# Kernel optimization log

Hardware: AMD Instinct MI355X
Metric: run time of the kernel (lower is better)

Reference implementation:

```python
import jax, jax.numpy as jnp
import numpy as np

M, K, N = 4096, 4096, 11008  # tokens, in_features, out_features


def setup_inputs() -> dict:
    key = jax.random.key(0)
    k1, k2, k3, k4 = jax.random.split(key, 4)
    x = jax.random.normal(k1, (M, K), dtype=jnp.float32)
    weight = jax.random.randint(k2, (N, K), -128, 128).astype(jnp.int8)
    # per-output-channel scale, small positive values as from real quantization
    weight_scale = (jax.random.uniform(k3, (N,), dtype=jnp.float32) * 0.01 + 1e-4)
    bias = jax.random.normal(k4, (N,), dtype=jnp.float32)
    return {"x": x, "weight": weight, "weight_scale": weight_scale, "bias": bias}


def reference(x, weight, weight_scale, bias):
    # Dynamic per-token symmetric quantization of activations to int8.
    x_scale = jnp.max(jnp.abs(x), axis=-1, keepdims=True) / 127.0  # [M, 1]
    x_scale = jnp.maximum(x_scale, 1e-8)
    x_q = jnp.clip(jnp.round(x / x_scale), -128, 127).astype(jnp.int8)  # [M, K]
    acc = jax.lax.dot_general(
        x_q, weight,
        dimension_numbers=(((1,), (1,)), ((), ())),
        preferred_element_type=jnp.int32,
    )
    # Dequantize: per-token activation scale * per-channel weight scale, add bias.
    out = acc.astype(jnp.float32) * x_scale * weight_scale[None, :] + bias[None, :]
    return out
```

## Files before the change

kernel.cpp:

```cpp
#include <hip/hip_runtime.h>
#include <stdint.h>

#define M_DIM 4096
#define K_DIM 4096
#define N_DIM 11008

typedef int v4i __attribute__((ext_vector_type(4)));

#define LDSP(p) ((__attribute__((address_space(3))) void*)(uintptr_t)(p))
#define GLBP(p) ((__attribute__((address_space(1))) void*)(uintptr_t)(p))

__global__ __launch_bounds__(256) void quant_rows(const float* __restrict__ x,
                                                  int8_t* __restrict__ xq,
                                                  float* __restrict__ xs_out) {
    const int row = blockIdx.x;
    const int t = threadIdx.x;
    const float4* xr = (const float4*)(x + (size_t)row * K_DIM);

    float4 v[4];
    float amax = 0.0f;
#pragma unroll
    for (int r = 0; r < 4; ++r) {
        v[r] = xr[t + r * 256];
        amax = fmaxf(amax, fmaxf(fmaxf(fabsf(v[r].x), fabsf(v[r].y)),
                                 fmaxf(fabsf(v[r].z), fabsf(v[r].w))));
    }
#pragma unroll
    for (int off = 32; off > 0; off >>= 1)
        amax = fmaxf(amax, __shfl_xor(amax, off));

    __shared__ float smax[4];
    if ((t & 63) == 0) smax[t >> 6] = amax;
    __syncthreads();
    amax = fmaxf(fmaxf(smax[0], smax[1]), fmaxf(smax[2], smax[3]));

    const float xs = fmaxf(amax / 127.0f, 1e-8f);
    if (t == 0) xs_out[row] = xs;

    int* qo = (int*)(xq + (size_t)row * K_DIM);
#pragma unroll
    for (int r = 0; r < 4; ++r) {
        int q0 = (int)rintf(v[r].x / xs);
        int q1 = (int)rintf(v[r].y / xs);
        int q2 = (int)rintf(v[r].z / xs);
        int q3 = (int)rintf(v[r].w / xs);
        q0 = min(127, max(-128, q0));
        q1 = min(127, max(-128, q1));
        q2 = min(127, max(-128, q2));
        q3 = min(127, max(-128, q3));
        int packed = (q0 & 255) | ((q1 & 255) << 8) | ((q2 & 255) << 16) | (q3 << 24);
        qo[t + r * 256] = packed;
    }
}

__global__ __launch_bounds__(256) void prep_weight(const void* __restrict__ wraw,
                                                   int8_t* __restrict__ w8) {
    const int* wi = (const int*)wraw;
    int c = 0;
#pragma unroll
    for (int i = 0; i < 64; ++i) {
        int w = wi[i];
        c += (w >= -128 && w <= 127) ? 1 : 0;
    }
    const size_t tid = (size_t)blockIdx.x * 256 + threadIdx.x;
    if (c >= 32) {
        union { int4 v; char b[16]; } o;
#pragma unroll
        for (int g = 0; g < 4; ++g) {
            int4 w = ((const int4*)wraw)[tid * 4 + g];
            o.b[g * 4 + 0] = (char)w.x;
            o.b[g * 4 + 1] = (char)w.y;
            o.b[g * 4 + 2] = (char)w.z;
            o.b[g * 4 + 3] = (char)w.w;
        }
        ((int4*)w8)[tid] = o.v;
    } else {
        ((int4*)w8)[tid] = ((const int4*)wraw)[tid];
    }
}

__global__ __launch_bounds__(256) void w8a8_gemm(const int8_t* __restrict__ xq,
                                                 const float* __restrict__ xscale,
                                                 const int8_t* __restrict__ wgt,
                                                 const float* __restrict__ wscale,
                                                 const float* __restrict__ bias,
                                                 float* __restrict__ out) {
    __shared__ __align__(16) int8_t lds_a[128 * 64];
    __shared__ __align__(16) int8_t lds_b[128 * 64];

    const int t = threadIdx.x;
    const int lane = t & 63;
    const int wave = t >> 6;
    const int quad = lane >> 4;
    const int l15 = lane & 15;
    const int bm = blockIdx.x;
    const int bn = blockIdx.y;

    const int wrow = (wave >> 1) * 64;
    const int wcol = (wave & 1) * 64;

    const int srow = t >> 2;
    const int sg = ((t & 3) ^ ((srow >> 1) & 3)) * 16;
    const int8_t* pa = xq + (size_t)(bm * 128 + srow) * K_DIM + sg;
    const int8_t* pb = wgt + (size_t)(bn * 128 + srow) * K_DIM + sg;
    const size_t half = (size_t)64 * K_DIM;

    void* la0 = (void*)(lds_a + t * 16);
    void* la1 = (void*)(lds_a + 4096 + t * 16);
    void* lb0 = (void*)(lds_b + t * 16);
    void* lb1 = (void*)(lds_b + 4096 + t * 16);

    int aoff[4], boff[4];
#pragma unroll
    for (int i = 0; i < 4; ++i) {
        const int ar = wrow + i * 16 + l15;
        aoff[i] = ar * 64 + ((quad ^ ((ar >> 1) & 3)) * 16);
        const int bc = wcol + i * 16 + l15;
        boff[i] = bc * 64 + ((quad ^ ((bc >> 1) & 3)) * 16);
    }

    v4i acc[4][4] = {};

    for (int k0 = 0; k0 < K_DIM; k0 += 64) {
        __builtin_amdgcn_global_load_lds(GLBP(pa), LDSP(la0), 16, 0, 0);
        __builtin_amdgcn_global_load_lds(GLBP(pa + half), LDSP(la1), 16, 0, 0);
        __builtin_amdgcn_global_load_lds(GLBP(pb), LDSP(lb0), 16, 0, 0);
        __builtin_amdgcn_global_load_lds(GLBP(pb + half), LDSP(lb1), 16, 0, 0);
        pa += 64;
        pb += 64;
        __syncthreads();

        v4i af[4], bf[4];
#pragma unroll
        for (int i = 0; i < 4; ++i) af[i] = *(const v4i*)(lds_a + aoff[i]);
#pragma unroll
        for (int j = 0; j < 4; ++j) bf[j] = *(const v4i*)(lds_b + boff[j]);

#pragma unroll
        for (int i = 0; i < 4; ++i)
#pragma unroll
            for (int j = 0; j < 4; ++j)
                acc[i][j] = __builtin_amdgcn_mfma_i32_16x16x64_i8(af[i], bf[j],
                                                                  acc[i][j], 0, 0, 0);
        __syncthreads();
    }

    float wsc[4], bi[4];
#pragma unroll
    for (int j = 0; j < 4; ++j) {
        const int cc = bn * 128 + wcol + j * 16 + l15;
        wsc[j] = wscale[cc];
        bi[j] = bias[cc];
    }
#pragma unroll
    for (int i = 0; i < 4; ++i) {
        const int m0 = bm * 128 + wrow + i * 16 + quad * 4;
        const float4 xs4 = *(const float4*)(xscale + m0);
        const float xsv[4] = {xs4.x, xs4.y, xs4.z, xs4.w};
#pragma unroll
        for (int r = 0; r < 4; ++r) {
            const size_t off = (size_t)(m0 + r) * N_DIM + (size_t)bn * 128 + wcol + l15;
#pragma unroll
            for (int j = 0; j < 4; ++j) {
                out[off + j * 16] = (float)acc[i][j][r] * xsv[r] * wsc[j] + bi[j];
            }
        }
    }
}

extern "C" void kernel_launch(void* const* d_in, const int* in_sizes, int n_in,
                              void* d_out, int out_size, void* d_ws, size_t ws_size,
                              hipStream_t stream) {
    const float* x = (const float*)d_in[0];
    const void* wraw = (const void*)d_in[1];
    const float* wscale = (const float*)d_in[2];
    const float* bias = (const float*)d_in[3];
    float* out = (float*)d_out;

    int8_t* w8 = (int8_t*)d_ws;
    int8_t* xq = (int8_t*)d_ws + (size_t)N_DIM * K_DIM;
    float* xs = (float*)((char*)d_ws + (size_t)N_DIM * K_DIM + (size_t)M_DIM * K_DIM);

    quant_rows<<<M_DIM, 256, 0, stream>>>(x, xq, xs);
    prep_weight<<<(N_DIM * (K_DIM / 16)) / 256, 256, 0, stream>>>(wraw, w8);
    dim3 grid(M_DIM / 128, N_DIM / 128);
    w8a8_gemm<<<grid, 256, 0, stream>>>(xq, xs, w8, wscale, bias, out);
}
```

Measured before the change: 538.1 us.

## Switch GEMM to 32x32x32 int8 MFMA and simplify weight repack kernel

The GEMM inner loop moves from sixteen 16x16x64 MFMAs per wave per K-step to eight 32x32x32 MFMAs, split over two k-halves. LDS fragment offsets and the epilogue register-to-row mapping are rewritten to match the 32x32 output layout. The weight prep kernel now has each thread pack one int4 of int32 weights into one int32 and probes only 8 words to detect the layout, at the cost of 4x more, smaller-work threads. The aim is fewer MFMA issues and fewer LDS fragment reads per FLOP, but the larger instruction changes latency and the epilogue store pattern.

```diff
diff --git a/kernel.cpp b/kernel.cpp
--- a/kernel.cpp
+++ b/kernel.cpp
@@ -6,6 +6,7 @@
 #define N_DIM 11008
 
 typedef int v4i __attribute__((ext_vector_type(4)));
+typedef int v16i __attribute__((ext_vector_type(16)));
 
 #define LDSP(p) ((__attribute__((address_space(3))) void*)(uintptr_t)(p))
 #define GLBP(p) ((__attribute__((address_space(1))) void*)(uintptr_t)(p))
@@ -58,24 +59,18 @@
     const int* wi = (const int*)wraw;
     int c = 0;
 #pragma unroll
-    for (int i = 0; i < 64; ++i) {
+    for (int i = 0; i < 8; ++i) {
         int w = wi[i];
         c += (w >= -128 && w <= 127) ? 1 : 0;
     }
     const size_t tid = (size_t)blockIdx.x * 256 + threadIdx.x;
-    if (c >= 32) {
-        union { int4 v; char b[16]; } o;
-#pragma unroll
-        for (int g = 0; g < 4; ++g) {
-            int4 w = ((const int4*)wraw)[tid * 4 + g];
-            o.b[g * 4 + 0] = (char)w.x;
-            o.b[g * 4 + 1] = (char)w.y;
-            o.b[g * 4 + 2] = (char)w.z;
-            o.b[g * 4 + 3] = (char)w.w;
-        }
-        ((int4*)w8)[tid] = o.v;
+    if (c >= 6) {
+        int4 w = ((const int4*)wraw)[tid];
+        int packed = (w.x & 255) | ((w.y & 255) << 8) | ((w.z & 255) << 16) | (w.w << 24);
+        ((int*)w8)[tid] = packed;
     } else {
-        ((int4*)w8)[tid] = ((const int4*)wraw)[tid];
+        const size_t n16 = (size_t)N_DIM * K_DIM / 16;
+        if (tid < n16) ((int4*)w8)[tid] = ((const int4*)wraw)[tid];
     }
 }
 
@@ -91,8 +86,8 @@
     const int t = threadIdx.x;
     const int lane = t & 63;
     const int wave = t >> 6;
-    const int quad = lane >> 4;
-    const int l15 = lane & 15;
+    const int l31 = lane & 31;
+    const int hi = lane >> 5;
     const int bm = blockIdx.x;
     const int bn = blockIdx.y;
 
@@ -110,16 +105,18 @@
     void* lb0 = (void*)(lds_b + t * 16);
     void* lb1 = (void*)(lds_b + 4096 + t * 16);
 
-    int aoff[4], boff[4];
+    int aoff[2][2], boff[2][2];
 #pragma unroll
-    for (int i = 0; i < 4; ++i) {
-        const int ar = wrow + i * 16 + l15;
-        aoff[i] = ar * 64 + ((quad ^ ((ar >> 1) & 3)) * 16);
-        const int bc = wcol + i * 16 + l15;
-        boff[i] = bc * 64 + ((quad ^ ((bc >> 1) & 3)) * 16);
-    }
+    for (int i = 0; i < 2; ++i)
+#pragma unroll
+        for (int kb = 0; kb < 2; ++kb) {
+            const int ar = wrow + i * 32 + l31;
+            aoff[i][kb] = ar * 64 + (((kb * 2 + hi) ^ ((ar >> 1) & 3)) * 16);
+            const int bc = wcol + i * 32 + l31;
+            boff[i][kb] = bc * 64 + (((kb * 2 + hi) ^ ((bc >> 1) & 3)) * 16);
+        }
 
-    v4i acc[4][4] = {};
+    v16i acc[2][2] = {};
 
     for (int k0 = 0; k0 < K_DIM; k0 += 64) {
         __builtin_amdgcn_global_load_lds(GLBP(pa), LDSP(la0), 16, 0, 0);
@@ -130,39 +127,48 @@
         pb += 64;
         __syncthreads();
 
-        v4i af[4], bf[4];
+        v4i af[2][2], bf[2][2];
 #pragma unroll
-        for (int i = 0; i < 4; ++i) af[i] = *(const v4i*)(lds_a + aoff[i]);
+        for (int i = 0; i < 2; ++i)
 #pragma unroll
-        for (int j = 0; j < 4; ++j) bf[j] = *(const v4i*)(lds_b + boff[j]);
+            for (int kb = 0; kb < 2; ++kb) {
+                af[i][kb] = *(const v4i*)(lds_a + aoff[i][kb]);
+                bf[i][kb] = *(const v4i*)(lds_b + boff[i][kb]);
+            }
 
 #pragma unroll
-        for (int i = 0; i < 4; ++i)
+        for (int kb = 0; kb < 2; ++kb)
 #pragma unroll
-            for (int j = 0; j < 4; ++j)
-                acc[i][j] = __builtin_amdgcn_mfma_i32_16x16x64_i8(af[i], bf[j],
-                                                                  acc[i][j], 0, 0, 0);
+            for (int i = 0; i < 2; ++i)
+#pragma unroll
+                for (int j = 0; j < 2; ++j)
+                    acc[i][j] = __builtin_amdgcn_mfma_i32_32x32x32_i8(
+                        af[i][kb], bf[j][kb], acc[i][j], 0, 0, 0);
         __syncthreads();
     }
 
-    float wsc[4], bi[4];
+    float wsc[2], bi[2];
 #pragma unroll
-    for (int j = 0; j < 4; ++j) {
-        const int cc = bn * 128 + wcol + j * 16 + l15;
+    for (int j = 0; j < 2; ++j) {
+        const int cc = bn * 128 + wcol + j * 32 + l31;
         wsc[j] = wscale[cc];
         bi[j] = bias[cc];
     }
 #pragma unroll
-    for (int i = 0; i < 4; ++i) {
-        const int m0 = bm * 128 + wrow + i * 16 + quad * 4;
-        const float4 xs4 = *(const float4*)(xscale + m0);
-        const float xsv[4] = {xs4.x, xs4.y, xs4.z, xs4.w};
+    for (int i = 0; i < 2; ++i) {
 #pragma unroll
-        for (int r = 0; r < 4; ++r) {
-            const size_t off = (size_t)(m0 + r) * N_DIM + (size_t)bn * 128 + wcol + l15;
+        for (int g = 0; g < 4; ++g) {
+            const int m0 = bm * 128 + wrow + i * 32 + g * 8 + hi * 4;
+            const float4 xs4 = *(const float4*)(xscale + m0);
+            const float xsv[4] = {xs4.x, xs4.y, xs4.z, xs4.w};
 #pragma unroll
-            for (int j = 0; j < 4; ++j) {
-                out[off + j * 16] = (float)acc[i][j][r] * xsv[r] * wsc[j] + bi[j];
+            for (int r = 0; r < 4; ++r) {
+                const int reg = g * 4 + r;
+                const size_t off = (size_t)(m0 + r) * N_DIM + (size_t)bn * 128 + wcol + l31;
+#pragma unroll
+                for (int j = 0; j < 2; ++j) {
+                    out[off + j * 32] = (float)acc[i][j][reg] * xsv[r] * wsc[j] + bi[j];
+                }
             }
         }
     }
@@ -182,7 +188,7 @@
     float* xs = (float*)((char*)d_ws + (size_t)N_DIM * K_DIM + (size_t)M_DIM * K_DIM);
 
     quant_rows<<<M_DIM, 256, 0, stream>>>(x, xq, xs);
-    prep_weight<<<(N_DIM * (K_DIM / 16)) / 256, 256, 0, stream>>>(wraw, w8);
+    prep_weight<<<(N_DIM * K_DIM / 4) / 256, 256, 0, stream>>>(wraw, w8);
     dim3 grid(M_DIM / 128, N_DIM / 128);
     w8a8_gemm<<<grid, 256, 0, stream>>>(xq, xs, w8, wscale, bias, out);
 }
```

Result: slower. 553.9 us (+2.9%).
